# Optimization experiments

Measured on AMD Instinct MI355X. Metric: run time of the kernel, lower is better.

The kernel has to match this reference:

```python
import jax, jax.numpy as jnp
import numpy as np

B, T, N, H = 256, 128, 1024, 1024


def setup_inputs() -> dict:
    key = jax.random.key(0)
    ks = jax.random.split(key, 7)
    s = 0.05
    return {
        "input_data": jax.random.normal(ks[0], (B, T, N), jnp.float32),
        "W_ih": jax.random.normal(ks[1], (4 * H, N), jnp.float32) * s,
        "W_hh": jax.random.normal(ks[2], (4 * H, H), jnp.float32) * s,
        "b_ih": jax.random.normal(ks[3], (4 * H,), jnp.float32) * s,
        "b_hh": jax.random.normal(ks[4], (4 * H,), jnp.float32) * s,
        "attn_w": jax.random.normal(ks[5], (2 * H + T,), jnp.float32) * s,
        "attn_b": jax.random.normal(ks[6], (1,), jnp.float32) * s,
    }


def reference(input_data, W_ih, W_hh, b_ih, b_hh, attn_w, attn_b):
    # input_data: [B, T, N]; torch LSTM gate order i, f, g, o.
    Bsz, Tn, Nn = input_data.shape
    Hn = W_hh.shape[1]
    # Decompose the attn linear over the concat [h, c, x_hist]:
    # score = h @ w_h + c @ w_c + x_perm @ w_x + b  (exactly the original Linear)
    w_h, w_c, w_x = attn_w[:Hn], attn_w[Hn:2 * Hn], attn_w[2 * Hn:]
    x_perm = jnp.transpose(input_data, (0, 2, 1))            # [B, N, T]
    score_x = x_perm @ w_x + attn_b[0]                        # [B, N], constant over t

    def step(carry, x_t):
        h, c = carry                                          # [B, H] each
        score = (h @ w_h + c @ w_c)[:, None] + score_x        # [B, N]
        a = jax.nn.softmax(score, axis=1)                     # [B, N]
        w_in = a * x_t                                        # weighted input [B, N]
        gates = w_in @ W_ih.T + b_ih + h @ W_hh.T + b_hh      # [B, 4H]
        i, f, g, o = jnp.split(gates, 4, axis=1)
        c_new = jax.nn.sigmoid(f) * c + jax.nn.sigmoid(i) * jnp.tanh(g)
        h_new = jax.nn.sigmoid(o) * jnp.tanh(c_new)
        return (h_new, c_new), (w_in, h_new)

    h0 = jnp.zeros((Bsz, Hn), input_data.dtype)
    c0 = jnp.zeros((Bsz, Hn), input_data.dtype)
    xs = jnp.transpose(input_data, (1, 0, 2))                 # [T, B, N]
    _, (iw, ie) = jax.lax.scan(step, (h0, c0), xs)
    input_weighted = jnp.transpose(iw, (1, 0, 2))             # [B, T, N]
    input_encoded = jnp.transpose(ie, (1, 0, 2))              # [B, T, H]
    return input_weighted, input_encoded
```

## Files before the change

kernel.cpp:

```cpp
#include <hip/hip_runtime.h>
#include <hip/hip_bf16.h>

#define BB 256
#define TT 128
#define NN 1024
#define HH 1024
#define G4 4096

typedef __attribute__((ext_vector_type(4))) float f32x4;
typedef __attribute__((ext_vector_type(8))) short bf16x8;

__device__ __forceinline__ unsigned short f2bf(float f) {
    unsigned int u = __builtin_bit_cast(unsigned int, f);
    u += 0x7FFFu + ((u >> 16) & 1u);
    return (unsigned short)(u >> 16);
}
__device__ __forceinline__ float bf2f(unsigned short s) {
    unsigned int u = ((unsigned int)s) << 16;
    return __builtin_bit_cast(float, u);
}

__global__ __launch_bounds__(512) void k_attn(
    const float* __restrict__ x, const float* __restrict__ attn_w,
    const float* __restrict__ attn_b, float* __restrict__ out0,
    unsigned short* __restrict__ win_bf)
{
    const int b = blockIdx.x;
    const int tid = threadIdx.x;
    const float* xb = x + (size_t)b * (TT * NN);
    const float* wx = attn_w + 2 * HH;

    float s0 = 0.f, s1 = 0.f;
    for (int t = 0; t < TT; ++t) {
        float2 v = *(const float2*)(xb + (size_t)t * NN + tid * 2);
        float w = wx[t];
        s0 += v.x * w; s1 += v.y * w;
    }
    float ab = attn_b[0];
    s0 += ab; s1 += ab;

    __shared__ float red[8];
    const int wv = tid >> 6, ln = tid & 63;
    float m = fmaxf(s0, s1);
#pragma unroll
    for (int off = 32; off > 0; off >>= 1) m = fmaxf(m, __shfl_xor(m, off));
    if (ln == 0) red[wv] = m;
    __syncthreads();
    m = red[0];
#pragma unroll
    for (int i = 1; i < 8; ++i) m = fmaxf(m, red[i]);

    float e0 = expf(s0 - m), e1 = expf(s1 - m);
    float sum = e0 + e1;
#pragma unroll
    for (int off = 32; off > 0; off >>= 1) sum += __shfl_xor(sum, off);
    __syncthreads();
    if (ln == 0) red[wv] = sum;
    __syncthreads();
    sum = 0.f;
#pragma unroll
    for (int i = 0; i < 8; ++i) sum += red[i];
    const float inv = 1.0f / sum;
    const float a0 = e0 * inv, a1 = e1 * inv;

    float* o = out0 + (size_t)b * (TT * NN);
    unsigned short* wb = win_bf + (size_t)b * (TT * NN);
    for (int t = 0; t < TT; ++t) {
        float2 v = *(const float2*)(xb + (size_t)t * NN + tid * 2);
        float2 w; w.x = a0 * v.x; w.y = a1 * v.y;
        *(float2*)(o + (size_t)t * NN + tid * 2) = w;
        unsigned int pk = (unsigned int)f2bf(w.x) | ((unsigned int)f2bf(w.y) << 16);
        *(unsigned int*)(wb + (size_t)t * NN + tid * 2) = pk;
    }
}

__global__ __launch_bounds__(256) void k_prep_w(
    const float* __restrict__ Wih, const float* __restrict__ Whh,
    const float* __restrict__ bih, const float* __restrict__ bhh,
    unsigned short* __restrict__ WihP, unsigned short* __restrict__ WhhP,
    float* __restrict__ biasP)
{
    const int p = blockIdx.x;
    const int j = p >> 2, g = p & 3;
    const int r = g * HH + j;
    const int tid = threadIdx.x;
    {
        float4 v = *(const float4*)(Wih + (size_t)r * NN + tid * 4);
        ushort4 o;
        o.x = f2bf(v.x); o.y = f2bf(v.y); o.z = f2bf(v.z); o.w = f2bf(v.w);
        *(ushort4*)(WihP + (size_t)p * NN + tid * 4) = o;
    }
    {
        float4 v = *(const float4*)(Whh + (size_t)r * HH + tid * 4);
        ushort4 o;
        o.x = f2bf(v.x); o.y = f2bf(v.y); o.z = f2bf(v.z); o.w = f2bf(v.w);
        *(ushort4*)(WhhP + (size_t)p * HH + tid * 4) = o;
    }
    if (tid == 0) biasP[p] = bih[r] + bhh[r];
}

__global__ __launch_bounds__(512, 1) void k_gemm_xp2(
    const unsigned short* __restrict__ A,
    const unsigned short* __restrict__ Bm,
    unsigned short* __restrict__ C)
{
    __shared__ unsigned short lA[3][4][256][8];
    __shared__ unsigned short lB[3][4][256][8];

    const int bid = blockIdx.x;
    const int cpx = gridDim.x >> 3;
    const int swz = (bid & 7) * cpx + (bid >> 3);
    const int NTN = G4 / 256;
    const int tm = swz / NTN, tn = swz % NTN;

    const int tid = threadIdx.x;
    const int wv = tid >> 6, ln = tid & 63;
    const int wm = wv >> 2, wn = wv & 3;
    const int rlo = ln & 15, khi = ln >> 4;

    const char* Ag = (const char*)A + (size_t)(tm * 256) * 2048;
    const char* Bg = (const char*)Bm + (size_t)(tn * 256) * 2048;

#define STAGE(buf_, c_) do { \
    _Pragma("unroll") \
    for (int j_ = 0; j_ < 2; ++j_) { \
        const int seg_ = (wv * 2 + j_) * 64 + ln; \
        const int khi_ = seg_ >> 8, row_ = seg_ & 255; \
        __builtin_amdgcn_global_load_lds( \
            (const __attribute__((address_space(1))) void*)(Ag + (size_t)row_ * 2048 + (c_) * 64 + khi_ * 16), \
            (__attribute__((address_space(3))) void*)((char*)&lA[buf_][0][0][0] + (wv * 2 + j_) * 1024), \
            16, 0, 0); \
        __builtin_amdgcn_global_load_lds( \
            (const __attribute__((address_space(1))) void*)(Bg + (size_t)row_ * 2048 + (c_) * 64 + khi_ * 16), \
            (__attribute__((address_space(3))) void*)((char*)&lB[buf_][0][0][0] + (wv * 2 + j_) * 1024), \
            16, 0, 0); \
    } } while (0)

    STAGE(0, 0); STAGE(1, 1); STAGE(2, 2);

    f32x4 acc[8][4] = {};

    for (int c = 0; c < 32; ++c) {
        const int buf = c % 3;
        if (c < 30)       { asm volatile("s_waitcnt vmcnt(8)" ::: "memory"); }
        else if (c == 30) { asm volatile("s_waitcnt vmcnt(4)" ::: "memory"); }
        else              { asm volatile("s_waitcnt vmcnt(0)" ::: "memory"); }
        __builtin_amdgcn_s_barrier();

        bf16x8 af[8], bfr[4];
#pragma unroll
        for (int m = 0; m < 8; ++m)
            af[m] = *(const bf16x8*)&lA[buf][khi][wm * 128 + m * 16 + rlo][0];
#pragma unroll
        for (int n = 0; n < 4; ++n)
            bfr[n] = *(const bf16x8*)&lB[buf][khi][wn * 64 + n * 16 + rlo][0];
        asm volatile("s_waitcnt lgkmcnt(0)" ::: "memory");
        __builtin_amdgcn_sched_barrier(0);
        __builtin_amdgcn_s_barrier();
        if (c < 29) STAGE(buf, c + 3);

        __builtin_amdgcn_s_setprio(1);
#pragma unroll
        for (int m = 0; m < 8; ++m)
#pragma unroll
            for (int n = 0; n < 4; ++n)
                acc[m][n] = __builtin_amdgcn_mfma_f32_16x16x32_bf16(af[m], bfr[n], acc[m][n], 0, 0, 0);
        __builtin_amdgcn_s_setprio(0);
    }
#undef STAGE

    const int rhi = ln >> 4;
#pragma unroll
    for (int m = 0; m < 8; ++m)
#pragma unroll
        for (int n = 0; n < 4; ++n)
#pragma unroll
            for (int j = 0; j < 4; ++j) {
                const int row = tm * 256 + wm * 128 + m * 16 + rhi * 4 + j;
                const int col = tn * 256 + wn * 64 + n * 16 + rlo;
                C[(size_t)row * G4 + col] = f2bf(acc[m][n][j]);
            }
}

__global__ __launch_bounds__(512) void k_step3(
    const int t,
    const unsigned short* __restrict__ hbf,
    const unsigned short* __restrict__ WhhP,
    const unsigned short* __restrict__ Xp,
    const float* __restrict__ biasP,
    float* __restrict__ cbuf,
    unsigned short* __restrict__ hbf_out,
    float* __restrict__ out1)
{
    __shared__ unsigned short lA[3][64 * 128];
    __shared__ unsigned short lB[3][64 * 128];
    __shared__ unsigned short lXp[64 * 64];

    const int bid = blockIdx.x;
    const int ti = bid >> 6, tj = bid & 63;
    const int tid = threadIdx.x;
    const int wv = tid >> 6, ln = tid & 63;
    const int wr = wv >> 1, wc = wv & 1;
    const int rlo = ln & 15, khi = ln >> 4;

    {
        const size_t bg = (size_t)(ti * 64 + wv * 8 + (ln >> 3));
        __builtin_amdgcn_global_load_lds(
            (const __attribute__((address_space(1))) void*)((const char*)Xp + ((bg * TT + t) << 13) + tj * 128 + (ln & 7) * 16),
            (__attribute__((address_space(3))) void*)((char*)lXp + wv * 1024),
            16, 0, 0);
    }

    const char* Ab = (const char*)hbf + (size_t)(ti * 64) * 2048;
    const char* Bb = (const char*)WhhP + (size_t)(tj * 64) * 2048;

#define STAGE(buf_, c_) do { \
    _Pragma("unroll") \
    for (int q_ = 0; q_ < 2; ++q_) { \
        const int r_ = q_ * 32 + wv * 4 + (ln >> 4); \
        const int so_ = (((ln & 15) ^ (r_ & 7)) << 4); \
        __builtin_amdgcn_global_load_lds( \
            (const __attribute__((address_space(1))) void*)(Ab + (size_t)r_ * 2048 + (c_) * 256 + so_), \
            (__attribute__((address_space(3))) void*)((char*)&lA[buf_][0] + q_ * 8192 + wv * 1024), \
            16, 0, 0); \
        __builtin_amdgcn_global_load_lds( \
            (const __attribute__((address_space(1))) void*)(Bb + (size_t)r_ * 2048 + (c_) * 256 + so_), \
            (__attribute__((address_space(3))) void*)((char*)&lB[buf_][0] + q_ * 8192 + wv * 1024), \
            16, 0, 0); \
    } } while (0)

    STAGE(0, 0);
    STAGE(1, 1);
    STAGE(2, 2);

    float4 bias4[2];
#pragma unroll
    for (int n = 0; n < 2; ++n)
        bias4[n] = *(const float4*)&biasP[(tj * 16 + wc * 8 + n * 4 + ((ln & 15) >> 2)) * 4];

    f32x4 acc[2] = {};

#pragma unroll
    for (int c = 0; c < 8; ++c) {
        const int buf = c % 3;
        if (c < 6)       { asm volatile("s_waitcnt vmcnt(8)" ::: "memory"); }
        else if (c == 6) { asm volatile("s_waitcnt vmcnt(4)" ::: "memory"); }
        else             { asm volatile("s_waitcnt vmcnt(0)" ::: "memory"); }
        __builtin_amdgcn_s_barrier();

        bf16x8 af[4], bfr[4][2];
#pragma unroll
        for (int kk = 0; kk < 4; ++kk) {
            {
                const int row = wr * 16 + rlo;
                const int off = (kk * 64 + khi * 16) ^ ((row & 7) << 4);
                af[kk] = *(const bf16x8*)((const char*)&lA[buf][0] + row * 256 + off);
            }
#pragma unroll
            for (int n = 0; n < 2; ++n) {
                const int row = wc * 32 + n * 16 + rlo;
                const int off = (kk * 64 + khi * 16) ^ ((row & 7) << 4);
                bfr[kk][n] = *(const bf16x8*)((const char*)&lB[buf][0] + row * 256 + off);
            }
        }
        asm volatile("s_waitcnt lgkmcnt(0)" ::: "memory");
        __builtin_amdgcn_sched_barrier(0);
        __builtin_amdgcn_s_barrier();
        if (c < 5) STAGE((c + 3) % 3, c + 3);
#pragma unroll
        for (int kk = 0; kk < 4; ++kk)
#pragma unroll
            for (int n = 0; n < 2; ++n)
                acc[n] = __builtin_amdgcn_mfma_f32_16x16x32_bf16(af[kk], bfr[kk][n], acc[n], 0, 0, 0);
    }
#undef STAGE

#pragma unroll
    for (int n = 0; n < 2; ++n) {
        f32x4 v = acc[n], u, w;
#pragma unroll
        for (int k = 0; k < 4; ++k) {
            float s = __shfl_xor(v[k ^ 1], 1);
            u[k] = ((k & 1) == (ln & 1)) ? v[k] : s;
        }
#pragma unroll
        for (int k = 0; k < 4; ++k) {
            float s = __shfl_xor(u[k ^ 2], 2);
            w[k] = (((k >> 1) & 1) == ((ln >> 1) & 1)) ? u[k] : s;
        }
        const int r_loc = wr * 16 + ((ln >> 4) << 2) + (ln & 3);
        const int u_loc = wc * 8 + n * 4 + ((ln & 15) >> 2);
        const ushort4 xp4 = *(const ushort4*)((const char*)lXp + r_loc * 128 + u_loc * 8);
        const float gi = w[0] + bf2f(xp4.x) + bias4[n].x;
        const float gf = w[1] + bf2f(xp4.y) + bias4[n].y;
        const float gg = w[2] + bf2f(xp4.z) + bias4[n].z;
        const float go = w[3] + bf2f(xp4.w) + bias4[n].w;
        const float i_ = 1.f / (1.f + expf(-gi));
        const float f_ = 1.f / (1.f + expf(-gf));
        const float g_ = tanhf(gg);
        const float o_ = 1.f / (1.f + expf(-go));
        const int bg = ti * 64 + r_loc;
        const int ug = tj * 16 + u_loc;
        const float cprev = cbuf[(size_t)bg * HH + ug];
        const float cc = f_ * cprev + i_ * g_;
        cbuf[(size_t)bg * HH + ug] = cc;
        const float h_ = o_ * tanhf(cc);
        out1[(size_t)bg * (TT * HH) + (size_t)t * HH + ug] = h_;
        hbf_out[(size_t)bg * HH + ug] = f2bf(h_);
    }
}

__global__ __launch_bounds__(256) void k_zero(float4* __restrict__ p)
{
    p[blockIdx.x * 256 + threadIdx.x] = make_float4(0.f, 0.f, 0.f, 0.f);
}

extern "C" void kernel_launch(void* const* d_in, const int* in_sizes, int n_in,
                              void* d_out, int out_size, void* d_ws, size_t ws_size,
                              hipStream_t stream)
{
    const float* x      = (const float*)d_in[0];
    const float* Wih    = (const float*)d_in[1];
    const float* Whh    = (const float*)d_in[2];
    const float* bih    = (const float*)d_in[3];
    const float* bhh    = (const float*)d_in[4];
    const float* attn_w = (const float*)d_in[5];
    const float* attn_b = (const float*)d_in[6];

    float* out0 = (float*)d_out;
    float* out1 = (float*)d_out + (size_t)BB * TT * NN;

    char* w = (char*)d_ws;
    unsigned short* WihP  = (unsigned short*)(w);
    unsigned short* WhhP  = (unsigned short*)(w + 8388608);
    float*          biasP = (float*)(w + 16777216);
    unsigned short* winbf = (unsigned short*)(w + 16793600);
    unsigned short* Xp    = (unsigned short*)(w + 83902464);
    unsigned short* hbf0  = (unsigned short*)(w + 352337920);
    unsigned short* hbf1  = (unsigned short*)(w + 352862208);
    float*          cbuf  = (float*)(w + 353386496);

    k_attn<<<BB, 512, 0, stream>>>(x, attn_w, attn_b, out0, winbf);
    k_prep_w<<<G4, 256, 0, stream>>>(Wih, Whh, bih, bhh, WihP, WhhP, biasP);
    k_gemm_xp2<<<(BB * TT / 256) * (G4 / 256), 512, 0, stream>>>(winbf, WihP, Xp);
    k_zero<<<512, 256, 0, stream>>>((float4*)hbf0);

    for (int t = 0; t < TT; ++t) {
        const unsigned short* hin = (t & 1) ? hbf1 : hbf0;
        unsigned short* hout      = (t & 1) ? hbf0 : hbf1;
        k_step3<<<256, 512, 0, stream>>>(t, hin, WhhP, Xp, biasP, cbuf, hout, out1);
    }
}
```

Baseline: 1.832 ms.

## Double K tile to 64 with XOR-swizzled LDS and double buffering in input GEMM

The precomputed input-projection GEMM now stages K-chunks of 64 bf16 elements instead of 32. It uses two LDS buffers instead of three and an XOR swizzle on the 16-byte segments so the fragment reads avoid bank conflicts. This halves the number of barrier and waitcnt iterations and doubles the MFMA work between synchronisations. In exchange the pipeline depth drops from three stages to two, so load latency may be hidden less well. LDS use goes from 96 KB to 128 KB per block.

```diff
diff --git a/kernel.cpp b/kernel.cpp
--- a/kernel.cpp
+++ b/kernel.cpp
@@ -99,13 +99,13 @@
     if (tid == 0) biasP[p] = bih[r] + bhh[r];
 }
 
-__global__ __launch_bounds__(512, 1) void k_gemm_xp2(
+__global__ __launch_bounds__(512, 1) void k_gemm_xp3(
     const unsigned short* __restrict__ A,
     const unsigned short* __restrict__ Bm,
     unsigned short* __restrict__ C)
 {
-    __shared__ unsigned short lA[3][4][256][8];
-    __shared__ unsigned short lB[3][4][256][8];
+    __shared__ unsigned short lA[2][256][64];
+    __shared__ unsigned short lB[2][256][64];
 
     const int bid = blockIdx.x;
     const int cpx = gridDim.x >> 3;
@@ -123,48 +123,59 @@
 
 #define STAGE(buf_, c_) do { \
     _Pragma("unroll") \
-    for (int j_ = 0; j_ < 2; ++j_) { \
-        const int seg_ = (wv * 2 + j_) * 64 + ln; \
-        const int khi_ = seg_ >> 8, row_ = seg_ & 255; \
+    for (int i_ = 0; i_ < 4; ++i_) { \
+        const int s_ = (wv * 4 + i_) * 64 + ln; \
+        const int r_ = s_ >> 3, j_ = s_ & 7; \
+        const size_t so_ = (size_t)r_ * 2048 + (size_t)(c_) * 128 + ((j_ ^ (r_ & 7)) << 4); \
         __builtin_amdgcn_global_load_lds( \
-            (const __attribute__((address_space(1))) void*)(Ag + (size_t)row_ * 2048 + (c_) * 64 + khi_ * 16), \
-            (__attribute__((address_space(3))) void*)((char*)&lA[buf_][0][0][0] + (wv * 2 + j_) * 1024), \
-            16, 0, 0); \
+            (const __attribute__((address_space(1))) void*)(Ag + so_), \
+            (__attribute__((address_space(3))) void*)((char*)&lA[buf_][0][0] + (wv * 4 + i_) * 1024), 16, 0, 0); \
         __builtin_amdgcn_global_load_lds( \
-            (const __attribute__((address_space(1))) void*)(Bg + (size_t)row_ * 2048 + (c_) * 64 + khi_ * 16), \
-            (__attribute__((address_space(3))) void*)((char*)&lB[buf_][0][0][0] + (wv * 2 + j_) * 1024), \
-            16, 0, 0); \
+            (const __attribute__((address_space(1))) void*)(Bg + so_), \
+            (__attribute__((address_space(3))) void*)((char*)&lB[buf_][0][0] + (wv * 4 + i_) * 1024), 16, 0, 0); \
     } } while (0)
 
-    STAGE(0, 0); STAGE(1, 1); STAGE(2, 2);
+    STAGE(0, 0); STAGE(1, 1);
 
     f32x4 acc[8][4] = {};
 
-    for (int c = 0; c < 32; ++c) {
-        const int buf = c % 3;
-        if (c < 30)       { asm volatile("s_waitcnt vmcnt(8)" ::: "memory"); }
-        else if (c == 30) { asm volatile("s_waitcnt vmcnt(4)" ::: "memory"); }
-        else              { asm volatile("s_waitcnt vmcnt(0)" ::: "memory"); }
+#pragma unroll 2
+    for (int c = 0; c < 16; ++c) {
+        const int buf = c & 1;
+        if (c < 15) { asm volatile("s_waitcnt vmcnt(8)" ::: "memory"); }
+        else        { asm volatile("s_waitcnt vmcnt(0)" ::: "memory"); }
         __builtin_amdgcn_s_barrier();
 
-        bf16x8 af[8], bfr[4];
-#pragma unroll
-        for (int m = 0; m < 8; ++m)
-            af[m] = *(const bf16x8*)&lA[buf][khi][wm * 128 + m * 16 + rlo][0];
-#pragma unroll
-        for (int n = 0; n < 4; ++n)
-            bfr[n] = *(const bf16x8*)&lB[buf][khi][wn * 64 + n * 16 + rlo][0];
+        bf16x8 af[2][8], bfr[2][4];
+#pragma unroll
+        for (int kk = 0; kk < 2; ++kk) {
+            const int sidx = kk * 4 + khi;
+#pragma unroll
+            for (int m = 0; m < 8; ++m) {
+                const int row = wm * 128 + m * 16 + rlo;
+                const int off = ((sidx ^ (row & 7)) << 4);
+                af[kk][m] = *(const bf16x8*)((const char*)&lA[buf][0][0] + row * 128 + off);
+            }
+#pragma unroll
+            for (int n = 0; n < 4; ++n) {
+                const int row = wn * 64 + n * 16 + rlo;
+                const int off = ((sidx ^ (row & 7)) << 4);
+                bfr[kk][n] = *(const bf16x8*)((const char*)&lB[buf][0][0] + row * 128 + off);
+            }
+        }
         asm volatile("s_waitcnt lgkmcnt(0)" ::: "memory");
         __builtin_amdgcn_sched_barrier(0);
         __builtin_amdgcn_s_barrier();
-        if (c < 29) STAGE(buf, c + 3);
+        if (c < 14) STAGE(buf, c + 2);
 
         __builtin_amdgcn_s_setprio(1);
 #pragma unroll
-        for (int m = 0; m < 8; ++m)
-#pragma unroll
-            for (int n = 0; n < 4; ++n)
-                acc[m][n] = __builtin_amdgcn_mfma_f32_16x16x32_bf16(af[m], bfr[n], acc[m][n], 0, 0, 0);
+        for (int kk = 0; kk < 2; ++kk)
+#pragma unroll
+            for (int m = 0; m < 8; ++m)
+#pragma unroll
+                for (int n = 0; n < 4; ++n)
+                    acc[m][n] = __builtin_amdgcn_mfma_f32_16x16x32_bf16(af[kk][m], bfr[kk][n], acc[m][n], 0, 0, 0);
         __builtin_amdgcn_s_setprio(0);
     }
 #undef STAGE
@@ -342,7 +353,7 @@
 
     k_attn<<<BB, 512, 0, stream>>>(x, attn_w, attn_b, out0, winbf);
     k_prep_w<<<G4, 256, 0, stream>>>(Wih, Whh, bih, bhh, WihP, WhhP, biasP);
-    k_gemm_xp2<<<(BB * TT / 256) * (G4 / 256), 512, 0, stream>>>(winbf, WihP, Xp);
+    k_gemm_xp3<<<(BB * TT / 256) * (G4 / 256), 512, 0, stream>>>(winbf, WihP, Xp);
     k_zero<<<512, 256, 0, stream>>>((float4*)hbf0);
 
     for (int t = 0; t < TT; ++t) {
```

Result: slower. 2.079 ms (+13.5%).
